# Kernel tuning notes

Hardware: AMD Instinct MI355X
Metric: run time of the kernel (lower is better)

## Reference

```python
import jax, jax.numpy as jnp
import numpy as np

B, N, T = 1, 1024, 2048   # batch, graph nodes, timesteps
E, K = 16384, 32          # edges, causal kernel taps


def setup_inputs() -> dict:
    key = jax.random.key(0)
    k1, k2, k3, k4 = jax.random.split(key, 4)
    x = jax.random.normal(k1, (B, N, T), dtype=jnp.float32)
    # per-edge causal impulse-response kernels (aggregator(g) output)
    kernel = jax.random.normal(k2, (E, K), dtype=jnp.float32) * 0.1
    src = jax.random.randint(k3, (E,), 0, N)
    dst = jax.random.randint(k4, (E,), 0, N)
    return {"x": x, "kernel": kernel, "src": src, "dst": dst}


def reference(x, kernel, src, dst):
    # Block-sparse causal conv over the edge list:
    #   y_e[b, t] = sum_k kernel[e, k] * x[b, src_e, t - k]   (causal)
    #   out[b, n, t] = x[b, n, t] + sum_{e: dst_e = n} y_e[b, t]
    # (residual applied because g.include_index_diag is False)
    xs = x[:, src, :]                      # [B, E, T] gather upstream signals
    rhs = kernel[:, None, ::-1]            # [E, 1, K] flipped -> true causal conv
    y = jax.lax.conv_general_dilated(
        xs, rhs,
        window_strides=(1,),
        padding=[(K - 1, 0)],              # left-pad: strictly causal
        dimension_numbers=("NCW", "OIW", "NCW"),
        feature_group_count=E,             # one independent kernel per edge
    )                                      # [B, E, T]
    agg = jax.ops.segment_sum(jnp.swapaxes(y, 0, 1), dst, num_segments=N)  # [N, B, T]
    return x + jnp.swapaxes(agg, 0, 1)     # [B, N, T]
```

## Files before the change

### kernel.cpp

```cpp
#include <hip/hip_runtime.h>
#include <hip/hip_bf16.h>

#define TT  2048
#define KK  32
#define NN  1024
#define EE  16384
#define CAP 64

typedef short short8  __attribute__((ext_vector_type(8)));
typedef short short4v __attribute__((ext_vector_type(4)));
typedef float f32x4   __attribute__((ext_vector_type(4)));

__device__ short g_xbf[NN * TT];
__device__ short g_kbf[EE * KK];

__device__ __forceinline__ short f2bf(float f) {
    __hip_bfloat16 h = __float2bfloat16(f);
    return __builtin_bit_cast(short, h);
}

__device__ __forceinline__ void gload_lds16(const short* g, short* l) {
    __builtin_amdgcn_global_load_lds(
        (const __attribute__((address_space(1))) void*)(const void*)(g),
        (__attribute__((address_space(3))) void*)(void*)(l), 16, 0, 0);
}

__global__ __launch_bounds__(256) void cvt_kernel(const float* __restrict__ x,
                                                  const float* __restrict__ kern,
                                                  int* __restrict__ cnt) {
    const int bid = blockIdx.x;
    if (bid < NN) {
        const int i = bid * 256 + threadIdx.x;
        const float4* x4 = (const float4*)x;
        const float4 a = x4[2 * i], b = x4[2 * i + 1];
        short8 h;
        h[0]=f2bf(a.x); h[1]=f2bf(a.y); h[2]=f2bf(a.z); h[3]=f2bf(a.w);
        h[4]=f2bf(b.x); h[5]=f2bf(b.y); h[6]=f2bf(b.z); h[7]=f2bf(b.w);
        ((short8*)g_xbf)[i] = h;
    } else if (bid < NN + 256) {
        const int i = (bid - NN) * 256 + threadIdx.x;
        const float4* k4 = (const float4*)kern;
        const float4 a = k4[2 * i], b = k4[2 * i + 1];
        short8 h;
        h[0]=f2bf(a.x); h[1]=f2bf(a.y); h[2]=f2bf(a.z); h[3]=f2bf(a.w);
        h[4]=f2bf(b.x); h[5]=f2bf(b.y); h[6]=f2bf(b.z); h[7]=f2bf(b.w);
        ((short8*)g_kbf)[i] = h;
    } else {
        int4* c4 = (int4*)cnt;
        c4[threadIdx.x] = make_int4(0, 0, 0, 0);
    }
}

__global__ __launch_bounds__(256) void csr_kernel(const int* __restrict__ src,
                                                  const int* __restrict__ dst,
                                                  int* __restrict__ cnt,
                                                  unsigned* __restrict__ slots) {
    const int e = blockIdx.x * 256 + threadIdx.x;
    const int d = dst[e];
    const int p = atomicAdd(&cnt[d], 1);
    if (p < CAP) slots[(size_t)d * CAP + p] = ((unsigned)src[e] << 14) | (unsigned)e;
}

__global__ __launch_bounds__(256, 6) void lti_kernel(
    const float*    __restrict__ x,
    const int*      __restrict__ cnt,
    const unsigned* __restrict__ slots,
    float*          __restrict__ out)
{
    const int bid = blockIdx.x;
    const int w   = bid >> 10;
    const int n   = bid & 1023;
    const int tid = threadIdx.x;
    const int q   = tid >> 6;
    const int ln  = tid & 63;
    const int c   = ln & 15, g = ln >> 4;
    const int t0  = 512 * w;

    __shared__ __align__(16) short xs_all[4][3][544];
    __shared__ __align__(16) short kt_all[4][8][72];
    __shared__ __align__(16) float red[4][512];
    __shared__ __align__(16) short dummy[32];
    __shared__ unsigned bl[CAP];

    short (*xsb)[544] = xs_all[q];
    short (*kt)[72]   = kt_all[q];

    short8 z8; z8[0]=0;z8[1]=0;z8[2]=0;z8[3]=0;z8[4]=0;z8[5]=0;z8[6]=0;z8[7]=0;

    {
        short8* kz = (short8*)&kt[0][0];
        kz[ln] = z8;
        if (ln < 8) kz[64 + ln] = z8;
        if (w == 0 && ln < 12) *(short8*)&xsb[ln >> 2][8 * (ln & 3)] = z8;
    }
    if (tid < CAP) bl[tid] = slots[(size_t)n * CAP + tid];
    int L = cnt[n]; if (L > CAP) L = CAP;
    __syncthreads();

    const int M = (L - q + 3) >> 2;
    #define IDX(I) (q + 4 * (I))

    f32x4 acc0 = {0,0,0,0}, acc1 = {0,0,0,0};
    short4v tr0, tr1, tr2;

    const int a_ = c & 7;
    const int s1 = ((a_ + 1) & 7) + 15 - c + 8 * g;

    #define ISSUE(S, P)                                                                \
    {                                                                                  \
        const unsigned sv = bl[P];                                                     \
        const int e0 = __builtin_amdgcn_readfirstlane((int)(sv & 16383u));             \
        const int s0 = __builtin_amdgcn_readfirstlane((int)(sv >> 14));                \
        const short* rb = g_xbf + (size_t)s0 * TT;                                     \
        gload_lds16(rb + t0 + 8 * ln, &xsb[S][32]);                                    \
        if (ln < 4)                                                                    \
            gload_lds16(rb + (w ? t0 - 32 : 0) + 8 * ln, w ? &xsb[S][0] : dummy);      \
        tr##S = *(const short4v*)(g_kbf + ((size_t)e0 << 5) + 4 * (ln & 7));           \
    }

    #define COMMIT(S)                                                                  \
    {                                                                                  \
        const int a2 = ln >> 3, pad = (a2 + 1) & 7, mb = 4 * (ln & 7);                 \
        kt[a2][pad + 47 - mb] = tr##S[0];                                              \
        kt[a2][pad + 46 - mb] = tr##S[1];                                              \
        kt[a2][pad + 45 - mb] = tr##S[2];                                              \
        kt[a2][pad + 44 - mb] = tr##S[3];                                              \
    }

    #define COMPUTE(S)                                                                 \
    {                                                                                  \
        const short8 b1 = *(const short8*)&kt[a_][s1];                                 \
        short8 b2 = *(const short8*)&kt[a_][s1 + 16];                                  \
        if (g < 2) b2 = z8;                              \
        {                                                                              \
            const short8 a1  = *(const short8*)&xsb[S][16 * c + 8 * g];                \
            const short8 a2v = *(const short8*)&xsb[S][16 * c + 8 * g + 16];           \
            acc0 = __builtin_amdgcn_mfma_f32_16x16x32_bf16(a1,  b1, acc0, 0, 0, 0);    \
            acc0 = __builtin_amdgcn_mfma_f32_16x16x32_bf16(a2v, b2, acc0, 0, 0, 0);    \
        }                                                                              \
        {                                                                              \
            const short8 a1  = *(const short8*)&xsb[S][256 + 16 * c + 8 * g];          \
            const short8 a2v = *(const short8*)&xsb[S][256 + 16 * c + 8 * g + 16];     \
            acc1 = __builtin_amdgcn_mfma_f32_16x16x32_bf16(a1,  b1, acc1, 0, 0, 0);    \
            acc1 = __builtin_amdgcn_mfma_f32_16x16x32_bf16(a2v, b2, acc1, 0, 0, 0);    \
        }                                                                              \
    }

    #define BODY(SC, SN, I)                                                            \
    if ((I) < M) {                                                                     \
        __builtin_amdgcn_sched_barrier(0);                                             \
        if ((I) + 2 < M) ISSUE(SN, IDX((I) + 2));                                      \
        const int rem = M - (I);                                                       \
        if (rem >= 3)      { asm volatile("s_waitcnt vmcnt(6)" ::: "memory"); }        \
        else if (rem == 2) { asm volatile("s_waitcnt vmcnt(3)" ::: "memory"); }        \
        else               { asm volatile("s_waitcnt vmcnt(0)" ::: "memory"); }        \
        __builtin_amdgcn_sched_barrier(0);                                             \
        COMMIT(SC);                                                                    \
        COMPUTE(SC);                                                                   \
    }

    if (M > 0) {
        ISSUE(0, IDX(0));
        if (M > 1) ISSUE(1, IDX(1));
        for (int i = 0; i < M; i += 3) {
            BODY(0, 2, i);
            BODY(1, 0, i + 1);
            BODY(2, 1, i + 2);
        }
    }

    {
        float* rd = &red[q][0];
        #pragma unroll
        for (int qd = 0; qd < 4; ++qd) {
            const int ta = 64 * g + 16 * qd + c;
            rd[ta]       = acc0[qd];
            rd[256 + ta] = acc1[qd];
        }
    }
    __syncthreads();
    {
        const int u = 2 * tid;
        const float2 r0 = *(const float2*)&red[0][u];
        const float2 r1 = *(const float2*)&red[1][u];
        const float2 r2 = *(const float2*)&red[2][u];
        const float2 r3 = *(const float2*)&red[3][u];
        const float2 xv = *(const float2*)(x + (size_t)n * TT + t0 + u);
        float2 o;
        o.x = xv.x + r0.x + r1.x + r2.x + r3.x;
        o.y = xv.y + r0.y + r1.y + r2.y + r3.y;
        *(float2*)(out + (size_t)n * TT + t0 + u) = o;
    }
    #undef IDX
    #undef ISSUE
    #undef COMMIT
    #undef COMPUTE
    #undef BODY
}

extern "C" void kernel_launch(void* const* d_in, const int* in_sizes, int n_in,
                              void* d_out, int out_size, void* d_ws, size_t ws_size,
                              hipStream_t stream) {
    const float* x    = (const float*)d_in[0];
    const float* kern = (const float*)d_in[1];
    const int*   src  = (const int*)d_in[2];
    const int*   dst  = (const int*)d_in[3];
    float*       out  = (float*)d_out;

    int*      cnt   = (int*)d_ws;
    unsigned* slots = (unsigned*)((char*)d_ws + 4096);

    cvt_kernel<<<dim3(NN + 256 + 1), dim3(256), 0, stream>>>(x, kern, cnt);
    csr_kernel<<<dim3(EE / 256), dim3(256), 0, stream>>>(src, dst, cnt, slots);
    lti_kernel<<<dim3(4 * NN), dim3(256), 0, stream>>>(x, cnt, slots, out);
}
```

Before: 42.16 us.

## Split time across waves per node and load bf16 x directly into registers

The lti kernel now uses one block per node, with each of the four waves covering a 512-sample time window, instead of four blocks per node that split edges across waves. This removes the LDS cross-wave reduction and its block barrier. The bf16 x copy is stored with a 32-sample zero left pad per row (row stride 2080), so MFMA operands can be loaded straight from global into registers rather than staged through LDS with global_load_lds. A two-stage register double buffer replaces the three-stage LDS pipeline. The trade-offs are fewer blocks (1024), a lower occupancy hint, and unaligned overlapping global loads that rely on cache reuse.

```diff
diff --git a/kernel.cpp b/kernel.cpp
--- a/kernel.cpp
+++ b/kernel.cpp
@@ -6,12 +6,13 @@
 #define NN  1024
 #define EE  16384
 #define CAP 64
+#define RS  2080
 
 typedef short short8  __attribute__((ext_vector_type(8)));
 typedef short short4v __attribute__((ext_vector_type(4)));
 typedef float f32x4   __attribute__((ext_vector_type(4)));
 
-__device__ short g_xbf[NN * TT];
+__device__ short g_xbf[NN * RS];
 __device__ short g_kbf[EE * KK];
 
 __device__ __forceinline__ short f2bf(float f) {
@@ -19,35 +20,31 @@
     return __builtin_bit_cast(short, h);
 }
 
-__device__ __forceinline__ void gload_lds16(const short* g, short* l) {
-    __builtin_amdgcn_global_load_lds(
-        (const __attribute__((address_space(1))) void*)(const void*)(g),
-        (__attribute__((address_space(3))) void*)(void*)(l), 16, 0, 0);
-}
-
 __global__ __launch_bounds__(256) void cvt_kernel(const float* __restrict__ x,
                                                   const float* __restrict__ kern,
                                                   int* __restrict__ cnt) {
-    const int bid = blockIdx.x;
+    const int bid = blockIdx.x, tid = threadIdx.x;
     if (bid < NN) {
-        const int i = bid * 256 + threadIdx.x;
-        const float4* x4 = (const float4*)x;
-        const float4 a = x4[2 * i], b = x4[2 * i + 1];
+        const float4* xr = (const float4*)(x + (size_t)bid * TT);
+        const float4 u = xr[2 * tid], v = xr[2 * tid + 1];
         short8 h;
-        h[0]=f2bf(a.x); h[1]=f2bf(a.y); h[2]=f2bf(a.z); h[3]=f2bf(a.w);
-        h[4]=f2bf(b.x); h[5]=f2bf(b.y); h[6]=f2bf(b.z); h[7]=f2bf(b.w);
-        ((short8*)g_xbf)[i] = h;
-    } else if (bid < NN + 256) {
-        const int i = (bid - NN) * 256 + threadIdx.x;
+        h[0]=f2bf(u.x); h[1]=f2bf(u.y); h[2]=f2bf(u.z); h[3]=f2bf(u.w);
+        h[4]=f2bf(v.x); h[5]=f2bf(v.y); h[6]=f2bf(v.z); h[7]=f2bf(v.w);
+        *(short8*)&g_xbf[(size_t)bid * RS + 32 + 8 * tid] = h;
+        if (tid < 4) {
+            short8 z; z[0]=0;z[1]=0;z[2]=0;z[3]=0;z[4]=0;z[5]=0;z[6]=0;z[7]=0;
+            *(short8*)&g_xbf[(size_t)bid * RS + 8 * tid] = z;
+        }
+    } else if (bid == NN) {
+        ((int4*)cnt)[tid] = make_int4(0, 0, 0, 0);
+    } else {
+        const int i = (bid - NN - 1) * 256 + tid;
         const float4* k4 = (const float4*)kern;
-        const float4 a = k4[2 * i], b = k4[2 * i + 1];
+        const float4 u = k4[2 * i], v = k4[2 * i + 1];
         short8 h;
-        h[0]=f2bf(a.x); h[1]=f2bf(a.y); h[2]=f2bf(a.z); h[3]=f2bf(a.w);
-        h[4]=f2bf(b.x); h[5]=f2bf(b.y); h[6]=f2bf(b.z); h[7]=f2bf(b.w);
+        h[0]=f2bf(u.x); h[1]=f2bf(u.y); h[2]=f2bf(u.z); h[3]=f2bf(u.w);
+        h[4]=f2bf(v.x); h[5]=f2bf(v.y); h[6]=f2bf(v.z); h[7]=f2bf(v.w);
         ((short8*)g_kbf)[i] = h;
-    } else {
-        int4* c4 = (int4*)cnt;
-        c4[threadIdx.x] = make_int4(0, 0, 0, 0);
     }
 }
 
@@ -61,29 +58,24 @@
     if (p < CAP) slots[(size_t)d * CAP + p] = ((unsigned)src[e] << 14) | (unsigned)e;
 }
 
-__global__ __launch_bounds__(256, 6) void lti_kernel(
+__global__ __launch_bounds__(256, 4) void lti_kernel(
     const float*    __restrict__ x,
     const int*      __restrict__ cnt,
     const unsigned* __restrict__ slots,
     float*          __restrict__ out)
 {
-    const int bid = blockIdx.x;
-    const int w   = bid >> 10;
-    const int n   = bid & 1023;
+    const int n   = blockIdx.x;
     const int tid = threadIdx.x;
-    const int q   = tid >> 6;
+    const int w   = tid >> 6;
     const int ln  = tid & 63;
     const int c   = ln & 15, g = ln >> 4;
     const int t0  = 512 * w;
+    const int D   = 16 * c + 8 * g;
 
-    __shared__ __align__(16) short xs_all[4][3][544];
     __shared__ __align__(16) short kt_all[4][8][72];
-    __shared__ __align__(16) float red[4][512];
-    __shared__ __align__(16) short dummy[32];
     __shared__ unsigned bl[CAP];
 
-    short (*xsb)[544] = xs_all[q];
-    short (*kt)[72]   = kt_all[q];
+    short (*kt)[72] = kt_all[w];
 
     short8 z8; z8[0]=0;z8[1]=0;z8[2]=0;z8[3]=0;z8[4]=0;z8[5]=0;z8[6]=0;z8[7]=0;
 
@@ -91,31 +83,29 @@
         short8* kz = (short8*)&kt[0][0];
         kz[ln] = z8;
         if (ln < 8) kz[64 + ln] = z8;
-        if (w == 0 && ln < 12) *(short8*)&xsb[ln >> 2][8 * (ln & 3)] = z8;
     }
     if (tid < CAP) bl[tid] = slots[(size_t)n * CAP + tid];
     int L = cnt[n]; if (L > CAP) L = CAP;
     __syncthreads();
 
-    const int M = (L - q + 3) >> 2;
-    #define IDX(I) (q + 4 * (I))
-
     f32x4 acc0 = {0,0,0,0}, acc1 = {0,0,0,0};
-    short4v tr0, tr1, tr2;
+    short8  xa0A, xb0A, xa1A, xb1A, xa0B, xb0B, xa1B, xb1B;
+    short4v trA, trB;
 
     const int a_ = c & 7;
     const int s1 = ((a_ + 1) & 7) + 15 - c + 8 * g;
 
-    #define ISSUE(S, P)                                                                \
+    #define LOADV(S, P)                                                                \
     {                                                                                  \
         const unsigned sv = bl[P];                                                     \
         const int e0 = __builtin_amdgcn_readfirstlane((int)(sv & 16383u));             \
         const int s0 = __builtin_amdgcn_readfirstlane((int)(sv >> 14));                \
-        const short* rb = g_xbf + (size_t)s0 * TT;                                     \
-        gload_lds16(rb + t0 + 8 * ln, &xsb[S][32]);                                    \
-        if (ln < 4)                                                                    \
-            gload_lds16(rb + (w ? t0 - 32 : 0) + 8 * ln, w ? &xsb[S][0] : dummy);      \
-        tr##S = *(const short4v*)(g_kbf + ((size_t)e0 << 5) + 4 * (ln & 7));           \
+        const short* rb = g_xbf + (size_t)s0 * RS + t0 + D;                            \
+        xa0##S = *(const short8*)(rb);                                                 \
+        xb0##S = *(const short8*)(rb + 16);                                            \
+        xa1##S = *(const short8*)(rb + 256);                                           \
+        xb1##S = *(const short8*)(rb + 272);                                           \
+        tr##S  = *(const short4v*)(g_kbf + ((size_t)e0 << 5) + 4 * (ln & 7));          \
     }
 
     #define COMMIT(S)                                                                  \
@@ -132,70 +122,35 @@
         const short8 b1 = *(const short8*)&kt[a_][s1];                                 \
         short8 b2 = *(const short8*)&kt[a_][s1 + 16];                                  \
         if (g < 2) b2 = z8;                              \
-        {                                                                              \
-            const short8 a1  = *(const short8*)&xsb[S][16 * c + 8 * g];                \
-            const short8 a2v = *(const short8*)&xsb[S][16 * c + 8 * g + 16];           \
-            acc0 = __builtin_amdgcn_mfma_f32_16x16x32_bf16(a1,  b1, acc0, 0, 0, 0);    \
-            acc0 = __builtin_amdgcn_mfma_f32_16x16x32_bf16(a2v, b2, acc0, 0, 0, 0);    \
-        }                                                                              \
-        {                                                                              \
-            const short8 a1  = *(const short8*)&xsb[S][256 + 16 * c + 8 * g];          \
-            const short8 a2v = *(const short8*)&xsb[S][256 + 16 * c + 8 * g + 16];     \
-            acc1 = __builtin_amdgcn_mfma_f32_16x16x32_bf16(a1,  b1, acc1, 0, 0, 0);    \
-            acc1 = __builtin_amdgcn_mfma_f32_16x16x32_bf16(a2v, b2, acc1, 0, 0, 0);    \
-        }                                                                              \
+        acc0 = __builtin_amdgcn_mfma_f32_16x16x32_bf16(xa0##S, b1, acc0, 0, 0, 0);     \
+        acc0 = __builtin_amdgcn_mfma_f32_16x16x32_bf16(xb0##S, b2, acc0, 0, 0, 0);     \
+        acc1 = __builtin_amdgcn_mfma_f32_16x16x32_bf16(xa1##S, b1, acc1, 0, 0, 0);     \
+        acc1 = __builtin_amdgcn_mfma_f32_16x16x32_bf16(xb1##S, b2, acc1, 0, 0, 0);     \
     }
 
-    #define BODY(SC, SN, I)                                                            \
-    if ((I) < M) {                                                                     \
-        __builtin_amdgcn_sched_barrier(0);                                             \
-        if ((I) + 2 < M) ISSUE(SN, IDX((I) + 2));                                      \
-        const int rem = M - (I);                                                       \
-        if (rem >= 3)      { asm volatile("s_waitcnt vmcnt(6)" ::: "memory"); }        \
-        else if (rem == 2) { asm volatile("s_waitcnt vmcnt(3)" ::: "memory"); }        \
-        else               { asm volatile("s_waitcnt vmcnt(0)" ::: "memory"); }        \
-        __builtin_amdgcn_sched_barrier(0);                                             \
-        COMMIT(SC);                                                                    \
-        COMPUTE(SC);                                                                   \
-    }
-
-    if (M > 0) {
-        ISSUE(0, IDX(0));
-        if (M > 1) ISSUE(1, IDX(1));
-        for (int i = 0; i < M; i += 3) {
-            BODY(0, 2, i);
-            BODY(1, 0, i + 1);
-            BODY(2, 1, i + 2);
+    if (L > 0) {
+        LOADV(A, 0);
+        if (L > 1) LOADV(B, 1);
+        for (int i = 0; i < L; i += 2) {
+            COMMIT(A);
+            COMPUTE(A);
+            if (i + 2 < L) LOADV(A, i + 2);
+            if (i + 1 < L) { COMMIT(B); COMPUTE(B); }
+            if (i + 3 < L) LOADV(B, i + 3);
         }
     }
 
-    {
-        float* rd = &red[q][0];
-        #pragma unroll
-        for (int qd = 0; qd < 4; ++qd) {
-            const int ta = 64 * g + 16 * qd + c;
-            rd[ta]       = acc0[qd];
-            rd[256 + ta] = acc1[qd];
-        }
+    const float* xr  = x   + (size_t)n * TT + t0;
+    float*       orw = out + (size_t)n * TT + t0;
+    #pragma unroll
+    for (int qd = 0; qd < 4; ++qd) {
+        const int ta = 64 * g + 16 * qd + c;
+        orw[ta]       = xr[ta]       + acc0[qd];
+        orw[256 + ta] = xr[256 + ta] + acc1[qd];
     }
-    __syncthreads();
-    {
-        const int u = 2 * tid;
-        const float2 r0 = *(const float2*)&red[0][u];
-        const float2 r1 = *(const float2*)&red[1][u];
-        const float2 r2 = *(const float2*)&red[2][u];
-        const float2 r3 = *(const float2*)&red[3][u];
-        const float2 xv = *(const float2*)(x + (size_t)n * TT + t0 + u);
-        float2 o;
-        o.x = xv.x + r0.x + r1.x + r2.x + r3.x;
-        o.y = xv.y + r0.y + r1.y + r2.y + r3.y;
-        *(float2*)(out + (size_t)n * TT + t0 + u) = o;
-    }
-    #undef IDX
-    #undef ISSUE
+    #undef LOADV
     #undef COMMIT
     #undef COMPUTE
-    #undef BODY
 }
 
 extern "C" void kernel_launch(void* const* d_in, const int* in_sizes, int n_in,
@@ -210,7 +165,7 @@
     int*      cnt   = (int*)d_ws;
     unsigned* slots = (unsigned*)((char*)d_ws + 4096);
 
-    cvt_kernel<<<dim3(NN + 256 + 1), dim3(256), 0, stream>>>(x, kern, cnt);
+    cvt_kernel<<<dim3(NN + 1 + EE * KK / 8 / 256), dim3(256), 0, stream>>>(x, kern, cnt);
     csr_kernel<<<dim3(EE / 256), dim3(256), 0, stream>>>(src, dst, cnt, slots);
-    lti_kernel<<<dim3(4 * NN), dim3(256), 0, stream>>>(x, cnt, slots, out);
+    lti_kernel<<<dim3(NN), dim3(256), 0, stream>>>(x, cnt, slots, out);
 }
```

Result: faster. 38.30 us (-9.1%).
